# Kernel optimization log

Hardware: AMD Instinct MI355X
Metric: run time of the kernel (lower is better)

Reference implementation:

```python
import jax, jax.numpy as jnp
import numpy as np
from jax.scipy.linalg import expm

# dims: batch B_, seq S_, d_inner Di, d_state Ds (must equal Di), dt_rank R
B_, S_, Di, Ds, R = 16, 512, 64, 64, 4


def setup_inputs() -> dict:
    key = jax.random.key(0)
    k0, k1, k2, k3 = jax.random.split(key, 4)
    x = jax.random.normal(k0, (B_, S_, Di), dtype=jnp.float32)
    # x_proj: Linear(Di -> R + 2*Ds); small init keeps dt small so expm stays finite
    Wx = jax.random.normal(k1, (R + 2 * Ds, Di), dtype=jnp.float32) * 0.05
    bx = jax.random.normal(k2, (R + 2 * Ds,), dtype=jnp.float32) * 0.05
    # dt_proj: Linear(R -> Di)
    Wdt = jax.random.normal(k3, (Di, R), dtype=jnp.float32) * 0.01
    bdt = jnp.zeros((Di,), dtype=jnp.float32)
    # A_log[d, n] = log(n+1), matching repeat(arange(1..Ds), 'n -> d n')
    A_log = jnp.log(jnp.broadcast_to(jnp.arange(1, Ds + 1, dtype=jnp.float32), (Di, Ds)))
    Dp = jnp.ones((Di,), dtype=jnp.float32)
    return {"x": x, "Wx": Wx, "bx": bx, "Wdt": Wdt, "bdt": bdt, "A_log": A_log, "Dp": Dp}


def _ssm_forward(x, Wx, bx, Wdt, bdt, A_log, Dp):
    b = x.shape[0]
    A = -jnp.exp(A_log)                    # (Di, Ds)
    I = jnp.eye(Di, Ds, dtype=x.dtype)     # (Di, Ds), square here
    expm_b = jax.vmap(expm)                # batched matrix exponential

    def step(hs, xi):
        # xi: (b, Di)
        proj = xi @ Wx.T + bx              # (b, R + 2*Ds)
        Bm = proj[:, :Ds]                  # (b, Ds)
        dtr = proj[:, Ds:Ds + R]           # (b, R)
        Cm = proj[:, Ds + R:]              # (b, Ds)
        dt = dtr @ Wdt.T + bdt             # (b, Di)
        deltaA = dt[:, :, None] * A[None]  # (b, Di, Ds) = diag(dt) @ A
        dA = expm_b(deltaA)                # exact discretization: exp(dt*A)
        deltaB = dt[:, :, None] * Bm[:, None, :]           # (b, Di, Ds)
        dB = jnp.linalg.pinv(deltaA) @ (dA - I) @ deltaB   # (dtA)^+ (e^{dtA}-I) dtB
        hs = hs * dA + xi[:, :, None] * dB
        mask = (jnp.abs(xi).sum(-1) > 1e-5).astype(x.dtype)[:, None, None]
        hs = hs * mask + jax.lax.stop_gradient(hs) * (1.0 - mask)
        hs = jnp.clip(hs, -1e6, 1e6)
        y = jnp.einsum('bdn,bn->bd', hs, Cm) + Dp * xi
        return hs, (y, hs)

    hs0 = jnp.zeros((b, Di, Ds), dtype=x.dtype)
    _, (ys, hss) = jax.lax.scan(step, hs0, jnp.swapaxes(x, 0, 1))
    # original returns (y of the LAST timestep, all hidden states (b, seq, Di, Ds))
    return ys[-1], jnp.swapaxes(hss, 0, 1)


def reference(x, Wx, bx, Wdt, bdt, A_log, Dp):
    return _ssm_forward(x, Wx, bx, Wdt, bdt, A_log, Dp)
```

## Files before the change

kernel.cpp:

```cpp
#include <hip/hip_runtime.h>
#include <cmath>

#define B_  16
#define S_  512
#define DI  64
#define DS  64
#define RR  4


__global__ __launch_bounds__(64)
void ssm_k1(const float* __restrict__ x, const float* __restrict__ Wx,
            const float* __restrict__ bx, const float* __restrict__ Wdt,
            const float* __restrict__ bdt, const float* __restrict__ A_log,
            float* __restrict__ ws)
{
    __shared__ float xs[DI];
    __shared__ float aa_s[DS];
    __shared__ float dtr_s[RR];
    const int bt   = blockIdx.x;
    const int lane = threadIdx.x;

    const float xv = x[bt * DI + lane];
    xs[lane]   = xv;
    aa_s[lane] = -expf(A_log[lane]);
    __syncthreads();

    float accB = bx[lane];
    {
        const float* wr = Wx + lane * DI;
        #pragma unroll
        for (int i = 0; i < DI; i += 4) {
            float4 w = *reinterpret_cast<const float4*>(wr + i);
            accB += w.x * xs[i] + w.y * xs[i + 1] + w.z * xs[i + 2] + w.w * xs[i + 3];
        }
    }
    if (lane < RR) {
        float acc = bx[DS + lane];
        const float* wr = Wx + (DS + lane) * DI;
        #pragma unroll
        for (int i = 0; i < DI; i += 4) {
            float4 w = *reinterpret_cast<const float4*>(wr + i);
            acc += w.x * xs[i] + w.y * xs[i + 1] + w.z * xs[i + 2] + w.w * xs[i + 3];
        }
        dtr_s[lane] = acc;
    }
    __syncthreads();

    float dtv = bdt[lane];
    #pragma unroll
    for (int r = 0; r < RR; ++r) dtv += dtr_s[r] * Wdt[lane * RR + r];

    const float a_l = aa_s[lane];

    float sv = a_l * dtv;
    float qv = a_l * a_l;
    #pragma unroll
    for (int off = 32; off > 0; off >>= 1) {
        sv += __shfl_xor(sv, off);
        qv += __shfl_xor(qv, off);
    }

    const float E   = expm1f(sv);
    const float phi = (fabsf(sv) < 1e-3f)
                        ? fmaf(sv, fmaf(sv, 1.0f / 6.0f, 0.5f), 1.0f)
                        : (E / sv);

    float* phidt = ws;
    float* uws   = ws + (size_t)B_ * S_ * DI;
    float* bmws  = ws + (size_t)2 * B_ * S_ * DI;

    phidt[bt * DI + lane] = phi * dtv;
    uws  [bt * DI + lane] = xv * (E / qv) * a_l;
    bmws [bt * DI + lane] = accB;

    if ((bt & (S_ - 1)) == (S_ - 1)) {
        float accC = bx[DS + RR + lane];
        const float* wr = Wx + (DS + RR + lane) * DI;
        #pragma unroll
        for (int i = 0; i < DI; i += 4) {
            float4 w = *reinterpret_cast<const float4*>(wr + i);
            accC += w.x * xs[i] + w.y * xs[i + 1] + w.z * xs[i + 2] + w.w * xs[i + 3];
        }
        float* cml = ws + (size_t)3 * B_ * S_ * DI;
        cml[(bt >> 9) * DS + lane] = accC;
    }
}

__global__ __launch_bounds__(256)
void ssm_k2(const float* __restrict__ ws, const float* __restrict__ x,
            const float* __restrict__ A_log, const float* __restrict__ Dp,
            float* __restrict__ out)
{
    const int tid  = threadIdx.x;
    const int n    = tid & 63;
    const int dsub = tid >> 6;
    const int b    = blockIdx.x >> 4;
    const int dg   = blockIdx.x & 15;
    const int d    = dg * 4 + dsub;

    const float a_n   = -expf(A_log[n]);
    const float delta = (d == n) ? 1.0f : 0.0f;

    const float* phidt = ws + (size_t)(b * S_) * DI + d;
    const float* uws   = ws + (size_t)B_ * S_ * DI + (size_t)(b * S_) * DI + d;
    const float* bmws  = ws + (size_t)2 * B_ * S_ * DI + (size_t)(b * S_) * DI + n;
    float* po = out + 1024 + (size_t)(b * S_) * (DI * DS) + d * DS + n;

    float h = 0.0f;
    #pragma unroll 16
    for (int t = 0; t < S_; ++t) {
        const float pv = phidt[t * DI];
        const float uv = uws[t * DI];
        const float bv = bmws[t * DI];
        const float av = fmaf(pv, a_n, delta);
        h = fmaf(av, h, uv * bv);
        h = fminf(fmaxf(h, -1.0e6f), 1.0e6f);
        po[(size_t)t * (DI * DS)] = h;
    }

    const float* cml = ws + (size_t)3 * B_ * S_ * DI;
    float v = h * cml[b * DS + n];
    #pragma unroll
    for (int off = 32; off > 0; off >>= 1) v += __shfl_xor(v, off);
    if (n == 0) {
        const float xi = x[((b * S_) + S_ - 1) * DI + d];
        out[b * DI + d] = v + Dp[d] * xi;
    }
}

extern "C" void kernel_launch(void* const* d_in, const int* in_sizes, int n_in,
                              void* d_out, int out_size, void* d_ws, size_t ws_size,
                              hipStream_t stream)
{
    const float* x     = (const float*)d_in[0];
    const float* Wx    = (const float*)d_in[1];
    const float* bx    = (const float*)d_in[2];
    const float* Wdt   = (const float*)d_in[3];
    const float* bdt   = (const float*)d_in[4];
    const float* A_log = (const float*)d_in[5];
    const float* Dp    = (const float*)d_in[6];
    float* out = (float*)d_out;
    float* ws  = (float*)d_ws;

    ssm_k1<<<B_ * S_, 64, 0, stream>>>(x, Wx, bx, Wdt, bdt, A_log, ws);
    ssm_k2<<<B_ * 16, 256, 0, stream>>>(ws, x, A_log, Dp, out);
}
```

Before: 62.41 us.

## Split sequential scan into chunked three-pass parallel scan with clamp-safe fallback

Replaces the single sequential 512-step scan kernel with a chunked scan. Pass one computes a per-chunk affine summary plus magnitude bounds, pass two combines chunk carries and falls back to a serial replay when the clamp could trigger, and pass three recomputes each chunk in parallel from its carry and writes all hidden states. This aims to raise parallelism from 256 blocks to 2048 so the latency-bound serial loop runs on more CUs. In exchange it adds two kernel launches, extra reads of the workspace inputs, and uses the output buffer as scratch for the summaries.

New measurement: 96.43 us. 54.5% more time.

```diff
diff --git a/kernel.cpp b/kernel.cpp
--- a/kernel.cpp
+++ b/kernel.cpp
@@ -6,7 +6,15 @@
 #define DI  64
 #define DS  64
 #define RR  4
-
+#define CH  8
+#define CL  64
+
+#define WS_U    524288
+#define WS_BM   1048576
+#define WS_CML  1572864
+#define WS_HIN  1573888
+
+#define SUMN 524288
 
 __global__ __launch_bounds__(64)
 void ssm_k1(const float* __restrict__ x, const float* __restrict__ Wx,
@@ -65,13 +73,9 @@
                         ? fmaf(sv, fmaf(sv, 1.0f / 6.0f, 0.5f), 1.0f)
                         : (E / sv);
 
-    float* phidt = ws;
-    float* uws   = ws + (size_t)B_ * S_ * DI;
-    float* bmws  = ws + (size_t)2 * B_ * S_ * DI;
-
-    phidt[bt * DI + lane] = phi * dtv;
-    uws  [bt * DI + lane] = xv * (E / qv) * a_l;
-    bmws [bt * DI + lane] = accB;
+    ws[bt * DI + lane]          = phi * dtv;
+    ws[WS_U + bt * DI + lane]   = xv * (E / qv) * a_l;
+    ws[WS_BM + bt * DI + lane]  = accB;
 
     if ((bt & (S_ - 1)) == (S_ - 1)) {
         float accC = bx[DS + RR + lane];
@@ -81,50 +85,136 @@
             float4 w = *reinterpret_cast<const float4*>(wr + i);
             accC += w.x * xs[i] + w.y * xs[i + 1] + w.z * xs[i + 2] + w.w * xs[i + 3];
         }
-        float* cml = ws + (size_t)3 * B_ * S_ * DI;
-        cml[(bt >> 9) * DS + lane] = accC;
+        ws[WS_CML + (bt >> 9) * DS + lane] = accC;
     }
 }
 
 __global__ __launch_bounds__(256)
-void ssm_k2(const float* __restrict__ ws, const float* __restrict__ x,
-            const float* __restrict__ A_log, const float* __restrict__ Dp,
-            float* __restrict__ out)
+void ssm_k2a(const float* __restrict__ ws, const float* __restrict__ A_log,
+             float* __restrict__ out)
 {
     const int tid  = threadIdx.x;
     const int n    = tid & 63;
-    const int dsub = tid >> 6;
-    const int b    = blockIdx.x >> 4;
-    const int dg   = blockIdx.x & 15;
-    const int d    = dg * 4 + dsub;
+    const int d    = ((blockIdx.x >> 3) & 15) * 4 + (tid >> 6);
+    const int c    = blockIdx.x & 7;
+    const int b    = blockIdx.x >> 7;
 
     const float a_n   = -expf(A_log[n]);
     const float delta = (d == n) ? 1.0f : 0.0f;
 
     const float* phidt = ws + (size_t)(b * S_) * DI + d;
-    const float* uws   = ws + (size_t)B_ * S_ * DI + (size_t)(b * S_) * DI + d;
-    const float* bmws  = ws + (size_t)2 * B_ * S_ * DI + (size_t)(b * S_) * DI + n;
+    const float* uws   = ws + WS_U + (size_t)(b * S_) * DI + d;
+    const float* bmws  = ws + WS_BM + (size_t)(b * S_) * DI + n;
+
+    const int t0 = c * CL;
+    float p = 1.0f, q = 0.0f, qa = 0.0f, Pm = 0.0f, Qm = 0.0f;
+    #pragma unroll 8
+    for (int j = 0; j < CL; ++j) {
+        const int t = t0 + j;
+        const float pv = phidt[(size_t)t * DI];
+        const float uv = uws[(size_t)t * DI];
+        const float bv = bmws[(size_t)t * DI];
+        const float av = fmaf(pv, a_n, delta);
+        const float w  = uv * bv;
+        p  = p * av;
+        q  = fmaf(av, q, w);
+        qa = fmaf(fabsf(av), qa, fabsf(w));
+        Pm = fmaxf(Pm, fabsf(p));
+        Qm = fmaxf(Qm, qa);
+    }
+    const size_t si = (((size_t)b * CH + c) * DI + d) * DS + n;
+    float* sum = out + 1024;
+    sum[si]            = p;
+    sum[SUMN + si]     = q;
+    sum[2 * SUMN + si] = Pm;
+    sum[3 * SUMN + si] = Qm;
+}
+
+__global__ __launch_bounds__(256)
+void ssm_k2b(float* __restrict__ ws, const float* __restrict__ out,
+             const float* __restrict__ A_log)
+{
+    const int tid = threadIdx.x;
+    const int n   = tid & 63;
+    const int d   = (blockIdx.x & 15) * 4 + (tid >> 6);
+    const int b   = blockIdx.x >> 4;
+
+    const float a_n   = -expf(A_log[n]);
+    const float delta = (d == n) ? 1.0f : 0.0f;
+
+    const float* sum   = out + 1024;
+    const float* phidt = ws + (size_t)(b * S_) * DI + d;
+    const float* uws   = ws + WS_U + (size_t)(b * S_) * DI + d;
+    const float* bmws  = ws + WS_BM + (size_t)(b * S_) * DI + n;
+    float* hin = ws + WS_HIN;
+
+    float h = 0.0f;
+    for (int c = 0; c < CH; ++c) {
+        const size_t si = (((size_t)b * CH + c) * DI + d) * DS + n;
+        hin[si] = h;
+        const float Pm = sum[2 * SUMN + si];
+        const float Qm = sum[3 * SUMN + si];
+        const float bound = fmaf(Pm, fabsf(h), Qm);
+        if (bound <= 1.0e6f) {
+            h = fmaf(sum[si], h, sum[SUMN + si]);
+            h = fminf(fmaxf(h, -1.0e6f), 1.0e6f);
+        } else {
+            const int t0 = c * CL;
+            #pragma unroll 8
+            for (int j = 0; j < CL; ++j) {
+                const int t = t0 + j;
+                const float av = fmaf(phidt[(size_t)t * DI], a_n, delta);
+                const float w  = uws[(size_t)t * DI] * bmws[(size_t)t * DI];
+                h = fmaf(av, h, w);
+                h = fminf(fmaxf(h, -1.0e6f), 1.0e6f);
+            }
+        }
+    }
+}
+
+__global__ __launch_bounds__(256)
+void ssm_k2c(const float* __restrict__ ws, const float* __restrict__ x,
+             const float* __restrict__ A_log, const float* __restrict__ Dp,
+             float* __restrict__ out)
+{
+    const int tid = threadIdx.x;
+    const int n   = tid & 63;
+    const int d   = ((blockIdx.x >> 3) & 15) * 4 + (tid >> 6);
+    const int c   = blockIdx.x & 7;
+    const int b   = blockIdx.x >> 7;
+
+    const float a_n   = -expf(A_log[n]);
+    const float delta = (d == n) ? 1.0f : 0.0f;
+
+    const float* phidt = ws + (size_t)(b * S_) * DI + d;
+    const float* uws   = ws + WS_U + (size_t)(b * S_) * DI + d;
+    const float* bmws  = ws + WS_BM + (size_t)(b * S_) * DI + n;
+
+    const size_t si = (((size_t)b * CH + c) * DI + d) * DS + n;
+    float h = ws[WS_HIN + si];
+
     float* po = out + 1024 + (size_t)(b * S_) * (DI * DS) + d * DS + n;
-
-    float h = 0.0f;
-    #pragma unroll 16
-    for (int t = 0; t < S_; ++t) {
-        const float pv = phidt[t * DI];
-        const float uv = uws[t * DI];
-        const float bv = bmws[t * DI];
+    const int t0 = c * CL;
+    #pragma unroll 8
+    for (int j = 0; j < CL; ++j) {
+        const int t = t0 + j;
+        const float pv = phidt[(size_t)t * DI];
+        const float uv = uws[(size_t)t * DI];
+        const float bv = bmws[(size_t)t * DI];
         const float av = fmaf(pv, a_n, delta);
         h = fmaf(av, h, uv * bv);
         h = fminf(fmaxf(h, -1.0e6f), 1.0e6f);
         po[(size_t)t * (DI * DS)] = h;
     }
 
-    const float* cml = ws + (size_t)3 * B_ * S_ * DI;
-    float v = h * cml[b * DS + n];
-    #pragma unroll
-    for (int off = 32; off > 0; off >>= 1) v += __shfl_xor(v, off);
-    if (n == 0) {
-        const float xi = x[((b * S_) + S_ - 1) * DI + d];
-        out[b * DI + d] = v + Dp[d] * xi;
+    if (c == CH - 1) {
+        float v = h * ws[WS_CML + b * DS + n];
+        #pragma unroll
+        for (int off = 32; off > 0; off >>= 1) v += __shfl_xor(v, off);
+        if (n == 0) {
+            const float xi = x[((b * S_) + S_ - 1) * DI + d];
+            out[b * DI + d] = v + Dp[d] * xi;
+        }
     }
 }
 
@@ -142,6 +232,8 @@
     float* out = (float*)d_out;
     float* ws  = (float*)d_ws;
 
-    ssm_k1<<<B_ * S_, 64, 0, stream>>>(x, Wx, bx, Wdt, bdt, A_log, ws);
-    ssm_k2<<<B_ * 16, 256, 0, stream>>>(ws, x, A_log, Dp, out);
-}
+    ssm_k1 <<<B_ * S_, 64, 0, stream>>>(x, Wx, bx, Wdt, bdt, A_log, ws);
+    ssm_k2a<<<B_ * 16 * CH, 256, 0, stream>>>(ws, A_log, out);
+    ssm_k2b<<<B_ * 16, 256, 0, stream>>>(ws, out, A_log);
+    ssm_k2c<<<B_ * 16 * CH, 256, 0, stream>>>(ws, x, A_log, Dp, out);
+}
```
